# Optimization experiments

Measured on AMD Instinct MI355X. Metric: run time of the kernel, lower is better.

The kernel has to match this reference:

```python
import jax, jax.numpy as jnp
import numpy as np

IN_FEATURES = 4096
OUT_FEATURES = 4096

def setup_inputs() -> dict:
    key = jax.random.key(0)
    kx, kw, kb = jax.random.split(key, 3)
    x = jax.random.normal(kx, (8192, IN_FEATURES), dtype=jnp.float32)
    weight = jax.random.normal(kw, (OUT_FEATURES, IN_FEATURES), dtype=jnp.float32)
    bias = jax.random.normal(kb, (OUT_FEATURES,), dtype=jnp.float32)
    return {"x": x, "weight": weight, "bias": bias}

def reference(x, weight, bias):
    # Binarize weights to {-1, 0, +1} via sign, then dense linear: y = x @ sign(W)^T + b
    w_bin = jnp.sign(weight)
    return jnp.einsum('bi,oi->bo', x, w_bin) + bias
```

## Files before the change

### kernel.cpp

```cpp
#include <hip/hip_runtime.h>
#include <hip/hip_bf16.h>
#include <stdint.h>

#define M_DIM 8192
#define N_DIM 4096
#define K_DIM 4096

#define NT 64

using i32x4 = __attribute__((ext_vector_type(4))) int;

typedef const __attribute__((address_space(1))) void glb_void_t;
typedef __attribute__((address_space(3))) void lds_void_t;

__device__ __forceinline__ void async16(const void* g, void* l) {
    __builtin_amdgcn_global_load_lds((glb_void_t*)(uintptr_t)g,
                                     (lds_void_t*)(uint32_t)(uintptr_t)l,
                                     16, 0, 0);
}

__device__ __forceinline__ int sgn_i8(float f) {
    union { float f; uint32_t u; } v; v.f = f;
    if ((v.u & 0x7FFFFFFFu) == 0u) return 0;
    return (v.u >> 31) ? -1 : 1;
}


__global__ void convert_w_kernel(const float* __restrict__ w,
                                 unsigned char* __restrict__ wq, int n4) {
    int stride = gridDim.x * blockDim.x;
    for (int i = blockIdx.x * blockDim.x + threadIdx.x; i < n4; i += stride) {
        float4 v = ((const float4*)w)[i];
        uint32_t o = ((uint32_t)(uint8_t)sgn_i8(v.x)) |
                     ((uint32_t)(uint8_t)sgn_i8(v.y) << 8) |
                     ((uint32_t)(uint8_t)sgn_i8(v.z) << 16) |
                     ((uint32_t)(uint8_t)sgn_i8(v.w) << 24);
        ((uint32_t*)wq)[i] = o;
    }
}


__global__ __launch_bounds__(256)
void convert_x_kernel(const float* __restrict__ x,
                      unsigned char* __restrict__ xq,
                      float* __restrict__ scales) {
    const int row = blockIdx.x;
    const int tid = threadIdx.x;
    const float4* xr = (const float4*)(x + (size_t)row * K_DIM);
    float4 v[4];
    float m = 0.f;
    #pragma unroll
    for (int j = 0; j < 4; ++j) {
        v[j] = xr[j * 256 + tid];
        m = fmaxf(m, fmaxf(fmaxf(fabsf(v[j].x), fabsf(v[j].y)),
                           fmaxf(fabsf(v[j].z), fabsf(v[j].w))));
    }
    #pragma unroll
    for (int off = 32; off >= 1; off >>= 1)
        m = fmaxf(m, __shfl_xor(m, off));
    __shared__ float wmax[4];
    if ((tid & 63) == 0) wmax[tid >> 6] = m;
    __syncthreads();
    m = fmaxf(fmaxf(wmax[0], wmax[1]), fmaxf(wmax[2], wmax[3]));
    const float inv = (m > 0.f) ? 127.0f / m : 0.f;
    if (tid == 0) scales[row] = (m > 0.f) ? m / 127.0f : 0.f;
    uint32_t* oq = (uint32_t*)(xq + (size_t)row * K_DIM);
    #pragma unroll
    for (int j = 0; j < 4; ++j) {
        float q0 = fminf(fmaxf(rintf(v[j].x * inv), -127.f), 127.f);
        float q1 = fminf(fmaxf(rintf(v[j].y * inv), -127.f), 127.f);
        float q2 = fminf(fmaxf(rintf(v[j].z * inv), -127.f), 127.f);
        float q3 = fminf(fmaxf(rintf(v[j].w * inv), -127.f), 127.f);
        uint32_t o = ((uint32_t)(uint8_t)(int)q0) |
                     ((uint32_t)(uint8_t)(int)q1 << 8) |
                     ((uint32_t)(uint8_t)(int)q2 << 16) |
                     ((uint32_t)(uint8_t)(int)q3 << 24);
        oq[j * 256 + tid] = o;
    }
}


#define BAR   __builtin_amdgcn_s_barrier()
#define VM4   asm volatile("s_waitcnt vmcnt(4)" ::: "memory")
#define VM0   asm volatile("s_waitcnt vmcnt(0)" ::: "memory")

#define STG(T) do { \
    const int pb_ = (T) & 3; \
    stage(pb_, 0, xq, brow,       (T) * 64); \
    stage(pb_, 1, xq, brow + 128, (T) * 64); \
    stage(pb_, 2, wq, bcol,       (T) * 64); \
    stage(pb_, 3, wq, bcol + 128, (T) * 64); \
} while (0)

#define RDSET(AV, BV, T) do { \
    const int rb_ = (T) & 3; \
    _Pragma("unroll") for (int nn = 0; nn < 4; ++nn) \
        BV[nn] = rdfrag(rb_, sectB, rB + nn * 16); \
    _Pragma("unroll") for (int mm = 0; mm < 8; ++mm) \
        AV[mm] = rdfrag(rb_, wm, mm * 16); \
} while (0)

#define MMA(AV, BV) do { \
    __builtin_amdgcn_s_setprio(1); \
    _Pragma("unroll") for (int mm = 0; mm < 8; ++mm) \
    _Pragma("unroll") for (int nn = 0; nn < 4; ++nn) \
        acc[mm][nn] = __builtin_amdgcn_mfma_i32_16x16x64_i8( \
            AV[mm], BV[nn], acc[mm][nn], 0, 0, 0); \
    __builtin_amdgcn_s_setprio(0); \
} while (0)

__global__ __launch_bounds__(512, 2)
void gemm_bin_kernel(const unsigned char* __restrict__ xq,
                     const unsigned char* __restrict__ wq,
                     const float* __restrict__ scales,
                     const float* __restrict__ bias,
                     float* __restrict__ out) {
    __shared__ __align__(16) unsigned char lds[4][4][8192];

    const int tid  = threadIdx.x;
    const int wid  = tid >> 6;
    const int lane = tid & 63;

    const int bid  = blockIdx.x;
    const int swzb = (bid & 7) * 64 + (bid >> 3);
    const int brow = (swzb >> 4) * 256;
    const int bcol = (swzb & 15) * 256;

    const int wm = wid >> 2;
    const int wn = wid & 3;
    const int fr  = lane & 15;
    const int g16 = (lane >> 4) << 4;
    const int sw  = ((lane >> 1) & 3) << 4;
    const int sectB = 2 + (wn >> 1);
    const int rB    = (wn & 1) * 64;

    i32x4 acc[8][4] = {};
    i32x4 a0[8], b0[4], a1[8], b1[4];

    const int srow = tid >> 2;
    const int scol = ((tid & 3) ^ ((tid >> 3) & 3)) * 16;
    auto stage = [&](int bufv, int sect, const unsigned char* g, int row0, int k0) {
        async16(g + (size_t)(row0 + srow) * K_DIM + (k0 + scol),
                &lds[bufv][sect][0] + tid * 16);
    };

    auto rdfrag = [&](int bufv, int sect, int rbase) -> i32x4 {
        const unsigned char* base = &lds[bufv][sect][0];
        return *(const i32x4*)(base + (rbase + fr) * 64 + (g16 ^ sw));
    };

    STG(0); STG(1); STG(2);
    VM4;
    BAR;
    RDSET(a0, b0, 0);

    for (int tt = 0; tt < 30; ++tt) {
        const int T = tt * 2;
        STG(T + 3); RDSET(a1, b1, T + 1); MMA(a0, b0); VM4; BAR;
        STG(T + 4); RDSET(a0, b0, T + 2); MMA(a1, b1); VM4; BAR;
    }
    STG(63); RDSET(a1, b1, 61); MMA(a0, b0); VM4; BAR;
    RDSET(a0, b0, 62); MMA(a1, b1); VM0; BAR;
    RDSET(a1, b1, 63); MMA(a0, b0);
    MMA(a1, b1);

    const int wrow = wm * 128, wcol = wn * 64;
    float bv[4];
    #pragma unroll
    for (int n = 0; n < 4; ++n) bv[n] = bias[bcol + wcol + n * 16 + fr];
    const int r4 = (lane >> 4) * 4;
    #pragma unroll
    for (int m = 0; m < 8; ++m) {
        #pragma unroll
        for (int rr = 0; rr < 4; ++rr) {
            const int row = brow + wrow + m * 16 + r4 + rr;
            const float sc = scales[row];
            float* orow = out + (size_t)row * N_DIM + bcol + wcol;
            #pragma unroll
            for (int n = 0; n < 4; ++n)
                orow[n * 16 + fr] = (float)acc[m][n][rr] * sc + bv[n];
        }
    }
}


__global__ void naive_kernel(const float* __restrict__ x,
                             const float* __restrict__ w,
                             const float* __restrict__ bias,
                             float* __restrict__ out) {
    const size_t total = (size_t)M_DIM * N_DIM;
    for (size_t idx = (size_t)blockIdx.x * blockDim.x + threadIdx.x; idx < total;
         idx += (size_t)gridDim.x * blockDim.x) {
        const size_t row = idx >> 12;
        const size_t col = idx & 4095;
        const float4* xr  = (const float4*)(x + row * K_DIM);
        const float4* wrp = (const float4*)(w + col * K_DIM);
        float s = 0.f;
        for (int k = 0; k < K_DIM / 4; ++k) {
            float4 a = xr[k], bq = wrp[k];
            s += a.x * (bq.x > 0.f ? 1.f : (bq.x < 0.f ? -1.f : 0.f));
            s += a.y * (bq.y > 0.f ? 1.f : (bq.y < 0.f ? -1.f : 0.f));
            s += a.z * (bq.z > 0.f ? 1.f : (bq.z < 0.f ? -1.f : 0.f));
            s += a.w * (bq.w > 0.f ? 1.f : (bq.w < 0.f ? -1.f : 0.f));
        }
        out[idx] = s + bias[col];
    }
}

extern "C" void kernel_launch(void* const* d_in, const int* in_sizes, int n_in,
                              void* d_out, int out_size, void* d_ws, size_t ws_size,
                              hipStream_t stream) {
    const float* x    = (const float*)d_in[0];
    const float* w    = (const float*)d_in[1];
    const float* bias = (const float*)d_in[2];
    float* out = (float*)d_out;

    const size_t xq_bytes = (size_t)M_DIM * K_DIM;
    const size_t wq_bytes = (size_t)N_DIM * K_DIM;
    const size_t sc_bytes = (size_t)M_DIM * sizeof(float);

    if (ws_size >= xq_bytes + wq_bytes + sc_bytes) {
        unsigned char* xq = (unsigned char*)d_ws;
        unsigned char* wq = (unsigned char*)d_ws + xq_bytes;
        float* scales     = (float*)((char*)d_ws + xq_bytes + wq_bytes);
        convert_w_kernel<<<2048, 256, 0, stream>>>(w, wq,
            (int)((size_t)N_DIM * K_DIM / 4));
        convert_x_kernel<<<M_DIM, 256, 0, stream>>>(x, xq, scales);
        gemm_bin_kernel<<<dim3((M_DIM / 256) * (N_DIM / 256)), dim3(512), 0, stream>>>(
            xq, wq, scales, bias, out);
    } else {
        naive_kernel<<<4096, 256, 0, stream>>>(x, w, bias, out);
    }
}
```

Before: 185.1 us.

## Pre-tile binarized weights and load B fragments directly from global into registers

The weight conversion kernel now writes sign bytes in a 64x64 tiled layout, so each wave can read its B fragments straight from global memory into registers instead of staging them through LDS. The LDS buffers shrink to hold only the activation tiles, and the A fragment LDS reads are interleaved with MFMA groups at raised priority. Explicit vmcnt waits inside the main loop are removed, so ordering now relies on waits the compiler inserts for the register loads. The cost is redundant B reads across the two waves that share a column block, global load latency sitting directly in the MFMA loop, and fragile synchronisation for the async LDS copies.

```diff
diff --git a/kernel.cpp b/kernel.cpp
--- a/kernel.cpp
+++ b/kernel.cpp
@@ -35,7 +35,12 @@
                      ((uint32_t)(uint8_t)sgn_i8(v.y) << 8) |
                      ((uint32_t)(uint8_t)sgn_i8(v.z) << 16) |
                      ((uint32_t)(uint8_t)sgn_i8(v.w) << 24);
-        ((uint32_t*)wq)[i] = o;
+        const int flat = i * 4;
+        const int row  = flat >> 12;
+        const int k    = flat & 4095;
+        const size_t dst = ((size_t)(row >> 6) << 18) + ((k >> 6) << 12) +
+                           ((row & 63) << 6) + (k & 63);
+        *(uint32_t*)(wq + dst) = o;
     }
 }
 
@@ -81,23 +86,23 @@
 
 
 #define BAR   __builtin_amdgcn_s_barrier()
-#define VM4   asm volatile("s_waitcnt vmcnt(4)" ::: "memory")
-#define VM0   asm volatile("s_waitcnt vmcnt(0)" ::: "memory")
-
-#define STG(T) do { \
+#define VM8   asm volatile("s_waitcnt vmcnt(8)" ::: "memory")
+
+#define STGA(T) do { \
     const int pb_ = (T) & 3; \
     stage(pb_, 0, xq, brow,       (T) * 64); \
     stage(pb_, 1, xq, brow + 128, (T) * 64); \
-    stage(pb_, 2, wq, bcol,       (T) * 64); \
-    stage(pb_, 3, wq, bcol + 128, (T) * 64); \
-} while (0)
-
-#define RDSET(AV, BV, T) do { \
+} while (0)
+
+#define BLOAD(BV, T) do { \
+    _Pragma("unroll") for (int nn = 0; nn < 4; ++nn) \
+        BV[nn] = *(const i32x4*)(bptr + (size_t)(T) * 4096 + nn * 1024); \
+} while (0)
+
+#define RDSETA(AV, T) do { \
     const int rb_ = (T) & 3; \
-    _Pragma("unroll") for (int nn = 0; nn < 4; ++nn) \
-        BV[nn] = rdfrag(rb_, sectB, rB + nn * 16); \
     _Pragma("unroll") for (int mm = 0; mm < 8; ++mm) \
-        AV[mm] = rdfrag(rb_, wm, mm * 16); \
+        AV[mm] = rdA(rb_, mm * 16); \
 } while (0)
 
 #define MMA(AV, BV) do { \
@@ -109,13 +114,36 @@
     __builtin_amdgcn_s_setprio(0); \
 } while (0)
 
+#define MM2(AV, BV, M0) \
+    _Pragma("unroll") for (int mm = (M0); mm < (M0) + 2; ++mm) \
+    _Pragma("unroll") for (int nn = 0; nn < 4; ++nn) \
+        acc[mm][nn] = __builtin_amdgcn_mfma_i32_16x16x64_i8( \
+            AV[mm], BV[nn], acc[mm][nn], 0, 0, 0);
+
+#define ITILE(CA, CB, NA, NB, T) do { \
+    const int rb_ = ((T) + 1) & 3; \
+    STGA((T) + 3); \
+    BLOAD(NB, (T) + 1); \
+    __builtin_amdgcn_s_setprio(1); \
+    NA[0] = rdA(rb_,  0); NA[1] = rdA(rb_, 16); \
+    MM2(CA, CB, 0) \
+    NA[2] = rdA(rb_, 32); NA[3] = rdA(rb_, 48); \
+    MM2(CA, CB, 2) \
+    NA[4] = rdA(rb_, 64); NA[5] = rdA(rb_, 80); \
+    MM2(CA, CB, 4) \
+    NA[6] = rdA(rb_, 96); NA[7] = rdA(rb_, 112); \
+    MM2(CA, CB, 6) \
+    __builtin_amdgcn_s_setprio(0); \
+    BAR; \
+} while (0)
+
 __global__ __launch_bounds__(512, 2)
 void gemm_bin_kernel(const unsigned char* __restrict__ xq,
                      const unsigned char* __restrict__ wq,
                      const float* __restrict__ scales,
                      const float* __restrict__ bias,
                      float* __restrict__ out) {
-    __shared__ __align__(16) unsigned char lds[4][4][8192];
+    __shared__ __align__(16) unsigned char lds[4][2][8192];
 
     const int tid  = threadIdx.x;
     const int wid  = tid >> 6;
@@ -131,8 +159,9 @@
     const int fr  = lane & 15;
     const int g16 = (lane >> 4) << 4;
     const int sw  = ((lane >> 1) & 3) << 4;
-    const int sectB = 2 + (wn >> 1);
-    const int rB    = (wn & 1) * 64;
+
+    const int nb = (bcol >> 6) + wn;
+    const unsigned char* bptr = wq + ((size_t)nb << 18) + fr * 64 + g16;
 
     i32x4 acc[8][4] = {};
     i32x4 a0[8], b0[4], a1[8], b1[4];
@@ -144,24 +173,25 @@
                 &lds[bufv][sect][0] + tid * 16);
     };
 
-    auto rdfrag = [&](int bufv, int sect, int rbase) -> i32x4 {
-        const unsigned char* base = &lds[bufv][sect][0];
+    auto rdA = [&](int bufv, int rbase) -> i32x4 {
+        const unsigned char* base = &lds[bufv][wm][0];
         return *(const i32x4*)(base + (rbase + fr) * 64 + (g16 ^ sw));
     };
 
-    STG(0); STG(1); STG(2);
-    VM4;
+    STGA(0); STGA(1); STGA(2);
+    BLOAD(b0, 0);
+    VM8;
     BAR;
-    RDSET(a0, b0, 0);
+    RDSETA(a0, 0);
 
     for (int tt = 0; tt < 30; ++tt) {
         const int T = tt * 2;
-        STG(T + 3); RDSET(a1, b1, T + 1); MMA(a0, b0); VM4; BAR;
-        STG(T + 4); RDSET(a0, b0, T + 2); MMA(a1, b1); VM4; BAR;
-    }
-    STG(63); RDSET(a1, b1, 61); MMA(a0, b0); VM4; BAR;
-    RDSET(a0, b0, 62); MMA(a1, b1); VM0; BAR;
-    RDSET(a1, b1, 63); MMA(a0, b0);
+        ITILE(a0, b0, a1, b1, T);
+        ITILE(a1, b1, a0, b0, T + 1);
+    }
+    ITILE(a0, b0, a1, b1, 60);
+    BLOAD(b0, 62); RDSETA(a0, 62); MMA(a1, b1); BAR;
+    BLOAD(b1, 63); RDSETA(a1, 63); MMA(a0, b0); BAR;
     MMA(a1, b1);
 
     const int wrow = wm * 128, wcol = wn * 64;
```

New measurement: 199.6 us. 1.08x slower.

## Switch int8 GEMM to 32x32x32 MFMA with interleaved LDS reads

Applied to the files above, without the earlier changes.

Replaces the 16x16x64 int8 MFMA tiling with 32x32x32 int8 MFMAs, so each wave holds 4x2 blocks of 16-lane accumulators and fragment reads index 32 rows across two K halves. The main loop gets a hand-interleaved ITILE that spreads the LDS fragment reads for the next tile between MFMA groups, with sched_group_barrier hints controlling the mix. The aim is fewer MFMA issues per tile and LDS latency hidden behind matrix math. The cost is a different accumulator layout and epilogue index mapping, and the scheduling hints may not be honored as intended.

```diff
diff --git a/kernel.cpp b/kernel.cpp
--- a/kernel.cpp
+++ b/kernel.cpp
@@ -8,7 +8,8 @@
 
 #define NT 64
 
-using i32x4 = __attribute__((ext_vector_type(4))) int;
+using i32x4  = __attribute__((ext_vector_type(4))) int;
+using i32x16 = __attribute__((ext_vector_type(16))) int;
 
 typedef const __attribute__((address_space(1))) void glb_void_t;
 typedef __attribute__((address_space(3))) void lds_void_t;
@@ -83,6 +84,8 @@
 #define BAR   __builtin_amdgcn_s_barrier()
 #define VM4   asm volatile("s_waitcnt vmcnt(4)" ::: "memory")
 #define VM0   asm volatile("s_waitcnt vmcnt(0)" ::: "memory")
+#define SGB_DS(N)   __builtin_amdgcn_sched_group_barrier(0x100, (N), 0)
+#define SGB_MFMA(N) __builtin_amdgcn_sched_group_barrier(0x008, (N), 0)
 
 #define STG(T) do { \
     const int pb_ = (T) & 3; \
@@ -94,19 +97,56 @@
 
 #define RDSET(AV, BV, T) do { \
     const int rb_ = (T) & 3; \
-    _Pragma("unroll") for (int nn = 0; nn < 4; ++nn) \
-        BV[nn] = rdfrag(rb_, sectB, rB + nn * 16); \
-    _Pragma("unroll") for (int mm = 0; mm < 8; ++mm) \
-        AV[mm] = rdfrag(rb_, wm, mm * 16); \
+    _Pragma("unroll") for (int kk = 0; kk < 2; ++kk) { \
+        _Pragma("unroll") for (int nn = 0; nn < 2; ++nn) \
+            BV[kk * 2 + nn] = rdfrag(rb_, sectB, rB + nn * 32, kk); \
+        _Pragma("unroll") for (int mm = 0; mm < 4; ++mm) \
+            AV[kk * 4 + mm] = rdfrag(rb_, wm, mm * 32, kk); \
+    } \
 } while (0)
 
 #define MMA(AV, BV) do { \
     __builtin_amdgcn_s_setprio(1); \
-    _Pragma("unroll") for (int mm = 0; mm < 8; ++mm) \
-    _Pragma("unroll") for (int nn = 0; nn < 4; ++nn) \
-        acc[mm][nn] = __builtin_amdgcn_mfma_i32_16x16x64_i8( \
-            AV[mm], BV[nn], acc[mm][nn], 0, 0, 0); \
+    _Pragma("unroll") for (int kk = 0; kk < 2; ++kk) \
+    _Pragma("unroll") for (int mm = 0; mm < 4; ++mm) \
+    _Pragma("unroll") for (int nn = 0; nn < 2; ++nn) \
+        acc[mm][nn] = __builtin_amdgcn_mfma_i32_32x32x32_i8( \
+            AV[kk * 4 + mm], BV[kk * 2 + nn], acc[mm][nn], 0, 0, 0); \
     __builtin_amdgcn_s_setprio(0); \
+} while (0)
+
+#define MM4(AV, BV, M0) \
+    _Pragma("unroll") for (int kk = 0; kk < 2; ++kk) \
+    _Pragma("unroll") for (int nn = 0; nn < 2; ++nn) \
+        acc[(M0)][nn] = __builtin_amdgcn_mfma_i32_32x32x32_i8( \
+            AV[kk * 4 + (M0)], BV[kk * 2 + nn], acc[(M0)][nn], 0, 0, 0);
+
+#define ITILE(CA, CB, NA, NB, T) do { \
+    const int rb_ = ((T) + 1) & 3; \
+    STG((T) + 3); \
+    __builtin_amdgcn_s_setprio(1); \
+    NB[0] = rdfrag(rb_, sectB, rB,      0); \
+    NB[1] = rdfrag(rb_, sectB, rB + 32, 0); \
+    NB[2] = rdfrag(rb_, sectB, rB,      1); \
+    MM4(CA, CB, 0) \
+    NB[3] = rdfrag(rb_, sectB, rB + 32, 1); \
+    NA[0] = rdfrag(rb_, wm,  0, 0); \
+    NA[4] = rdfrag(rb_, wm,  0, 1); \
+    MM4(CA, CB, 1) \
+    NA[1] = rdfrag(rb_, wm, 32, 0); \
+    NA[5] = rdfrag(rb_, wm, 32, 1); \
+    NA[2] = rdfrag(rb_, wm, 64, 0); \
+    MM4(CA, CB, 2) \
+    NA[6] = rdfrag(rb_, wm, 64, 1); \
+    NA[3] = rdfrag(rb_, wm, 96, 0); \
+    NA[7] = rdfrag(rb_, wm, 96, 1); \
+    MM4(CA, CB, 3) \
+    SGB_DS(3); SGB_MFMA(4); \
+    SGB_DS(3); SGB_MFMA(4); \
+    SGB_DS(3); SGB_MFMA(4); \
+    SGB_DS(3); SGB_MFMA(4); \
+    __builtin_amdgcn_s_setprio(0); \
+    VM4; BAR; \
 } while (0)
 
 __global__ __launch_bounds__(512, 2)
@@ -128,13 +168,13 @@
 
     const int wm = wid >> 2;
     const int wn = wid & 3;
-    const int fr  = lane & 15;
-    const int g16 = (lane >> 4) << 4;
+    const int l31 = lane & 31;
+    const int h16 = (lane >> 5) << 4;
     const int sw  = ((lane >> 1) & 3) << 4;
     const int sectB = 2 + (wn >> 1);
     const int rB    = (wn & 1) * 64;
 
-    i32x4 acc[8][4] = {};
+    i32x16 acc[4][2] = {};
     i32x4 a0[8], b0[4], a1[8], b1[4];
 
     const int srow = tid >> 2;
@@ -144,9 +184,9 @@
                 &lds[bufv][sect][0] + tid * 16);
     };
 
-    auto rdfrag = [&](int bufv, int sect, int rbase) -> i32x4 {
+    auto rdfrag = [&](int bufv, int sect, int rbase, int kk) -> i32x4 {
         const unsigned char* base = &lds[bufv][sect][0];
-        return *(const i32x4*)(base + (rbase + fr) * 64 + (g16 ^ sw));
+        return *(const i32x4*)(base + (rbase + l31) * 64 + ((kk * 32 + h16) ^ sw));
     };
 
     STG(0); STG(1); STG(2);
@@ -156,8 +196,8 @@
 
     for (int tt = 0; tt < 30; ++tt) {
         const int T = tt * 2;
-        STG(T + 3); RDSET(a1, b1, T + 1); MMA(a0, b0); VM4; BAR;
-        STG(T + 4); RDSET(a0, b0, T + 2); MMA(a1, b1); VM4; BAR;
+        ITILE(a0, b0, a1, b1, T);
+        ITILE(a1, b1, a0, b0, T + 1);
     }
     STG(63); RDSET(a1, b1, 61); MMA(a0, b0); VM4; BAR;
     RDSET(a0, b0, 62); MMA(a1, b1); VM0; BAR;
@@ -165,20 +205,23 @@
     MMA(a1, b1);
 
     const int wrow = wm * 128, wcol = wn * 64;
-    float bv[4];
-    #pragma unroll
-    for (int n = 0; n < 4; ++n) bv[n] = bias[bcol + wcol + n * 16 + fr];
-    const int r4 = (lane >> 4) * 4;
-    #pragma unroll
-    for (int m = 0; m < 8; ++m) {
+    const int h4 = (lane >> 5) * 4;
+    float bv[2];
+    #pragma unroll
+    for (int nb = 0; nb < 2; ++nb) bv[nb] = bias[bcol + wcol + nb * 32 + l31];
+    #pragma unroll
+    for (int mb = 0; mb < 4; ++mb) {
         #pragma unroll
-        for (int rr = 0; rr < 4; ++rr) {
-            const int row = brow + wrow + m * 16 + r4 + rr;
-            const float sc = scales[row];
-            float* orow = out + (size_t)row * N_DIM + bcol + wcol;
+        for (int rg = 0; rg < 4; ++rg) {
             #pragma unroll
-            for (int n = 0; n < 4; ++n)
-                orow[n * 16 + fr] = (float)acc[m][n][rr] * sc + bv[n];
+            for (int rr = 0; rr < 4; ++rr) {
+                const int row = brow + wrow + mb * 32 + rg * 8 + h4 + rr;
+                const float sc = scales[row];
+                float* orow = out + (size_t)row * N_DIM + bcol + wcol;
+                #pragma unroll
+                for (int nb = 0; nb < 2; ++nb)
+                    orow[nb * 32 + l31] = (float)acc[mb][nb][rg * 4 + rr] * sc + bv[nb];
+            }
         }
     }
 }
```

New measurement: 194.5 us. +5.0%, slower.
